# Performance work log

Hardware: AMD Instinct MI355X
Metric: run time of the kernel (lower is better)

## Reference

```python
import jax, jax.numpy as jnp
import numpy as np

DIM = 256
NUM_HEADS = 8
CHUNK = 64
EPS = 1e-5


def layernorm(x, g, b):
    m = jnp.mean(x, axis=-1, keepdims=True)
    v = jnp.mean((x - m) ** 2, axis=-1, keepdims=True)
    return (x - m) / jnp.sqrt(v + EPS) * g + b


def setup_inputs() -> dict:
    key = jax.random.key(0)
    ks = jax.random.split(key, 12)
    B, C, H, W = 8, DIM, 64, 64
    s = 1.0 / np.sqrt(C)
    return {
        "x": jax.random.normal(ks[0], (B, C, H, W), jnp.float32),
        "CVA_input": jax.random.normal(ks[1], (B, C, H, W), jnp.float32),
        "qn_g": jnp.ones((C,), jnp.float32), "qn_b": jnp.zeros((C,), jnp.float32),
        "kn_g": jnp.ones((C,), jnp.float32), "kn_b": jnp.zeros((C,), jnp.float32),
        "vn_g": jnp.ones((C,), jnp.float32), "vn_b": jnp.zeros((C,), jnp.float32),
        "Wq": jax.random.normal(ks[2], (C, C), jnp.float32) * s,
        "bq": jnp.zeros((C,), jnp.float32),
        "Wk": jax.random.normal(ks[3], (C, C), jnp.float32) * s,
        "bk": jnp.zeros((C,), jnp.float32),
        "Wv": jax.random.normal(ks[4], (C, C), jnp.float32) * s,
        "bv": jnp.zeros((C,), jnp.float32),
        "Wp": jax.random.normal(ks[5], (C, C), jnp.float32) * s,
        "bp": jnp.zeros((C,), jnp.float32),
    }


def reference(x, CVA_input, qn_g, qn_b, kn_g, kn_b, vn_g, vn_b,
              Wq, bq, Wk, bk, Wv, bv, Wp, bp):
    B, C, H, W = x.shape
    N = H * W
    nh = NUM_HEADS
    hd = C // nh
    scale = hd ** -0.5
    nc = N // CHUNK  # number of non-overlapping chunks

    xs = x.reshape(B, C, N).transpose(0, 2, 1)          # [B,N,C]
    cva = CVA_input.reshape(B, -1, C)                    # [B,N,C] (raw reshape, as in torch)

    def heads(t):  # [B,N,C] -> [B,nh,nc,CHUNK,hd]
        return t.reshape(B, N, nh, hd).transpose(0, 2, 1, 3).reshape(B, nh, nc, CHUNK, hd)

    q = heads(layernorm(cva, qn_g, qn_b) @ Wq + bq)
    k = heads(layernorm(cva, kn_g, kn_b) @ Wk + bk)
    v = heads(layernorm(xs, vn_g, vn_b) @ Wv + bv)

    # block-local attention: each chunk attends only within itself
    scores = jnp.einsum('bhncd,bhnkd->bhnck', q, k) * scale  # [B,nh,nc,CHUNK,CHUNK]
    probs = jax.nn.softmax(scores, axis=-1)
    o = jnp.einsum('bhnck,bhnkd->bhncd', probs, v)           # [B,nh,nc,CHUNK,hd]

    o = o.reshape(B, nh, N, hd).transpose(0, 2, 1, 3).reshape(B, N, C)
    out = o @ Wp + bp                                        # [B,N,C]
    return out.transpose(0, 2, 1).reshape(B, C, H, W)
```

## Files before the change

### kernel.cpp

```cpp
#include <hip/hip_runtime.h>
#include <hip/hip_bf16.h>

#define NTOK 4096
#define BATCH 8
#define NROWS (BATCH * NTOK)

typedef __attribute__((ext_vector_type(8))) short bfx8;
typedef __attribute__((ext_vector_type(4))) short bfx4;
typedef __attribute__((ext_vector_type(4))) float f32x4;

__device__ __forceinline__ short f2bf(float f) {
    unsigned u = __builtin_bit_cast(unsigned, f);
    u += 0x7fffu + ((u >> 16) & 1u);
    return (short)(u >> 16);
}
__device__ __forceinline__ unsigned pk2(float a, float b) {
    return (unsigned)(unsigned short)f2bf(a) | ((unsigned)(unsigned short)f2bf(b) << 16);
}

#define MFMA16(a, b, c) __builtin_amdgcn_mfma_f32_16x16x32_bf16(a, b, c, 0, 0, 0)
#define LGKM0()                                              \
    do {                                                     \
        asm volatile("s_waitcnt lgkmcnt(0)" ::: "memory");   \
        __builtin_amdgcn_sched_barrier(0);                   \
    } while (0)

__global__ __launch_bounds__(256) void prep_w(
    const float* __restrict__ Wq, const float* __restrict__ Wk,
    const float* __restrict__ Wv, const float* __restrict__ Wp,
    const float* __restrict__ qg, const float* __restrict__ qb,
    const float* __restrict__ kg, const float* __restrict__ kb,
    const float* __restrict__ vg, const float* __restrict__ vb,
    short* __restrict__ wt, float* __restrict__ bbp) {
    int m = blockIdx.x;
    int ci0 = blockIdx.y * 16;
    const float *W, *g, *be;
    float scale = 1.0f;
    if (m == 0)      { W = Wq; g = qg; be = qb; scale = 0.17677669529663687f; }
    else if (m == 1) { W = Wk; g = kg; be = kb; }
    else if (m == 2) { W = Wv; g = vg; be = vb; }
    else             { W = Wp; g = nullptr; be = nullptr; }
    __shared__ float tile[16][257];
    int t = threadIdx.x;
#pragma unroll
    for (int i = 0; i < 16; i++)
        tile[i][t] = W[(size_t)(ci0 + i) * 256 + t];
    __syncthreads();
    float p = 0.f;
    if (be) {
#pragma unroll
        for (int i = 0; i < 16; i++) p += be[ci0 + i] * tile[i][t];
    }
    bbp[(m * 16 + blockIdx.y) * 256 + t] = p;
    short* WT = wt + m * 65536 + t * 256 + ci0;
    bfx8 o0, o1;
#pragma unroll
    for (int j = 0; j < 8; j++) {
        float gv = g ? g[ci0 + j] : 1.0f;
        o0[j] = f2bf(scale * gv * tile[j][t]);
    }
#pragma unroll
    for (int j = 0; j < 8; j++) {
        float gv = g ? g[ci0 + 8 + j] : 1.0f;
        o1[j] = f2bf(scale * gv * tile[8 + j][t]);
    }
    *reinterpret_cast<bfx8*>(WT) = o0;
    *reinterpret_cast<bfx8*>(WT + 8) = o1;
}

__global__ __launch_bounds__(256) void prep_b(
    const float* __restrict__ bq, const float* __restrict__ bk,
    const float* __restrict__ bv, const float* __restrict__ bp,
    const float* __restrict__ bbp, float* __restrict__ bb) {
    int m = blockIdx.x, t = threadIdx.x;
    const float* bias = (m == 0) ? bq : (m == 1) ? bk : (m == 2) ? bv : bp;
    float scale = (m == 0) ? 0.17677669529663687f : 1.0f;
    float s = bias[t];
#pragma unroll
    for (int i = 0; i < 16; i++) s += bbp[(m * 16 + i) * 256 + t];
    bb[m * 256 + t] = scale * s;
}

__global__ __launch_bounds__(512, 4) void mega(const float* __restrict__ x,
                                               const float* __restrict__ cva,
                                               const short* __restrict__ wt,
                                               const float* __restrict__ bb,
                                               float* __restrict__ out) {
    int id = blockIdx.x;
    int b = id >> 6, ch = id & 63;
    int t = threadIdx.x, w = t >> 6, l = t & 63, c = l & 15, g = l >> 4;

    __shared__ short A[64 * 264];
    __shared__ short scr_[8][2560];
    __shared__ float red[8][64][2];
    short* S = scr_[w];

    const float* xb   = x + (size_t)b * 1048576 + ch * 64;
    const float* cvab = cva + (size_t)(b * 4096 + ch * 64) * 256;

    {
        int r16 = l >> 4;
        float fv[2][16];
#pragma unroll
        for (int p2 = 0; p2 < 2; p2++) {
            int row = w * 8 + p2 * 4 + r16;
#pragma unroll
            for (int i = 0; i < 4; i++) {
                float4 v4 = *reinterpret_cast<const float4*>(
                    cvab + (size_t)row * 256 + c * 16 + i * 4);
                fv[p2][i * 4 + 0] = v4.x;
                fv[p2][i * 4 + 1] = v4.y;
                fv[p2][i * 4 + 2] = v4.z;
                fv[p2][i * 4 + 3] = v4.w;
            }
        }
#pragma unroll
        for (int p2 = 0; p2 < 2; p2++) {
            int row = w * 8 + p2 * 4 + r16;
            float s = 0.f, q2 = 0.f;
#pragma unroll
            for (int i = 0; i < 16; i++) {
                s += fv[p2][i];
                q2 += fv[p2][i] * fv[p2][i];
            }
            s += __shfl_xor(s, 1);  q2 += __shfl_xor(q2, 1);
            s += __shfl_xor(s, 2);  q2 += __shfl_xor(q2, 2);
            s += __shfl_xor(s, 4);  q2 += __shfl_xor(q2, 4);
            s += __shfl_xor(s, 8);  q2 += __shfl_xor(q2, 8);
            float mean = s * (1.0f / 256.0f);
            float rstd = rsqrtf(q2 * (1.0f / 256.0f) - mean * mean + 1e-5f);
            bfx8 o0, o1;
#pragma unroll
            for (int jj = 0; jj < 8; jj++) {
                o0[jj] = f2bf((fv[p2][jj] - mean) * rstd);
                o1[jj] = f2bf((fv[p2][8 + jj] - mean) * rstd);
            }
            *reinterpret_cast<bfx8*>(A + row * 264 + c * 16) = o0;
            *reinterpret_cast<bfx8*>(A + row * 264 + c * 16 + 8) = o1;
        }
    }
    __syncthreads();

    f32x4 qa[4][2] = {}, ka[4][2] = {};
    {
        const short* wq0 = wt + (size_t)(w * 32 + c) * 256 + g * 8;
        const short* wq1 = wq0 + 16 * 256;
        const short* wk0 = wq0 + 65536;
        const short* wk1 = wq1 + 65536;
#pragma unroll
        for (int ks = 0; ks < 8; ks++) {
            bfx8 af[4];
#pragma unroll
            for (int m = 0; m < 4; m++)
                af[m] = *reinterpret_cast<const bfx8*>(A + (m * 16 + c) * 264 + ks * 32 + g * 8);
            bfx8 q0 = *reinterpret_cast<const bfx8*>(wq0 + ks * 32);
            bfx8 q1 = *reinterpret_cast<const bfx8*>(wq1 + ks * 32);
            bfx8 k0 = *reinterpret_cast<const bfx8*>(wk0 + ks * 32);
            bfx8 k1 = *reinterpret_cast<const bfx8*>(wk1 + ks * 32);
#pragma unroll
            for (int m = 0; m < 4; m++) {
                qa[m][0] = MFMA16(af[m], q0, qa[m][0]);
                qa[m][1] = MFMA16(af[m], q1, qa[m][1]);
                ka[m][0] = MFMA16(af[m], k0, ka[m][0]);
                ka[m][1] = MFMA16(af[m], k1, ka[m][1]);
            }
        }
    }

    float xg[32];
#pragma unroll
    for (int i = 0; i < 32; i++) xg[i] = xb[(size_t)(w * 32 + i) * 4096 + l];

    bfx8 qf[4];
    {
        float b0 = bb[w * 32 + c], b1 = bb[w * 32 + 16 + c];
#pragma unroll
        for (int m = 0; m < 4; m++)
#pragma unroll
            for (int j = 0; j < 4; j++) {
                S[(m * 16 + g * 4 + j) * 40 + c]      = f2bf(qa[m][0][j] + b0);
                S[(m * 16 + g * 4 + j) * 40 + 16 + c] = f2bf(qa[m][1][j] + b1);
            }
        LGKM0();
#pragma unroll
        for (int np = 0; np < 4; np++)
            qf[np] = *reinterpret_cast<const bfx8*>(S + (np * 16 + c) * 40 + g * 8);
        LGKM0();
    }

    bfx8 kf[4];
    {
        float b0 = bb[256 + w * 32 + c], b1 = bb[256 + w * 32 + 16 + c];
#pragma unroll
        for (int m = 0; m < 4; m++)
#pragma unroll
            for (int j = 0; j < 4; j++) {
                S[(m * 16 + g * 4 + j) * 40 + c]      = f2bf(ka[m][0][j] + b0);
                S[(m * 16 + g * 4 + j) * 40 + 16 + c] = f2bf(ka[m][1][j] + b1);
            }
        LGKM0();
#pragma unroll
        for (int m = 0; m < 4; m++)
            kf[m] = *reinterpret_cast<const bfx8*>(S + (m * 16 + c) * 40 + g * 8);
        LGKM0();
    }

    {
        float s = 0.f, q2 = 0.f;
#pragma unroll
        for (int i = 0; i < 32; i++) { s += xg[i]; q2 += xg[i] * xg[i]; }
        red[w][l][0] = s;
        red[w][l][1] = q2;
    }
    __syncthreads();

    float xmean, xrstd;
    {
        float s = 0.f, q2 = 0.f;
#pragma unroll
        for (int j2 = 0; j2 < 8; j2++) { s += red[j2][l][0]; q2 += red[j2][l][1]; }
        xmean = s * (1.0f / 256.0f);
        xrstd = rsqrtf(q2 * (1.0f / 256.0f) - xmean * xmean + 1e-5f);
    }

#pragma unroll
    for (int i2 = 0; i2 < 4; i2++) {
        bfx8 o;
#pragma unroll
        for (int jj = 0; jj < 8; jj++) o[jj] = f2bf((xg[i2 * 8 + jj] - xmean) * xrstd);
        *reinterpret_cast<bfx8*>(A + l * 264 + w * 32 + i2 * 8) = o;
    }
    __syncthreads();

    f32x4 sa[4][4] = {};
#pragma unroll
    for (int m = 0; m < 4; m++)
#pragma unroll
        for (int np = 0; np < 4; np++)
            sa[m][np] = MFMA16(kf[m], qf[np], sa[m][np]);

    float rs[4];
#pragma unroll
    for (int np = 0; np < 4; np++) {
        float mx = sa[0][np][0];
#pragma unroll
        for (int m = 0; m < 4; m++)
#pragma unroll
            for (int j = 0; j < 4; j++) mx = fmaxf(mx, sa[m][np][j]);
        mx = fmaxf(mx, __shfl_xor(mx, 16));
        mx = fmaxf(mx, __shfl_xor(mx, 32));
        float sum = 0.f;
#pragma unroll
        for (int m = 0; m < 4; m++)
#pragma unroll
            for (int j = 0; j < 4; j++) {
                float e = __expf(sa[m][np][j] - mx);
                sa[m][np][j] = e;
                sum += e;
            }
        sum += __shfl_xor(sum, 16);
        sum += __shfl_xor(sum, 32);
        rs[np] = 1.0f / sum;
    }

    unsigned Pp[4][4][2];
#pragma unroll
    for (int m = 0; m < 4; m++)
#pragma unroll
        for (int np = 0; np < 4; np++) {
            Pp[m][np][0] = pk2(sa[m][np][0], sa[m][np][1]);
            Pp[m][np][1] = pk2(sa[m][np][2], sa[m][np][3]);
        }

    f32x4 va[4][2] = {};
    {
        const short* w0 = wt + 2 * 65536 + (size_t)(w * 32 + c) * 256 + g * 8;
        const short* w1 = w0 + 16 * 256;
#pragma unroll
        for (int ks = 0; ks < 8; ks++) {
            bfx8 af[4];
#pragma unroll
            for (int m = 0; m < 4; m++)
                af[m] = *reinterpret_cast<const bfx8*>(A + (m * 16 + c) * 264 + ks * 32 + g * 8);
            bfx8 v0 = *reinterpret_cast<const bfx8*>(w0 + ks * 32);
            bfx8 v1 = *reinterpret_cast<const bfx8*>(w1 + ks * 32);
#pragma unroll
            for (int m = 0; m < 4; m++) {
                va[m][0] = MFMA16(af[m], v0, va[m][0]);
                va[m][1] = MFMA16(af[m], v1, va[m][1]);
            }
        }
    }
    __syncthreads();

    bfx8 vf[2][2];
    {
        float b0 = bb[512 + w * 32 + c], b1 = bb[512 + w * 32 + 16 + c];
#pragma unroll
        for (int m = 0; m < 4; m++) {
            bfx4 t0, t1;
#pragma unroll
            for (int j = 0; j < 4; j++) {
                t0[j] = f2bf(va[m][0][j] + b0);
                t1[j] = f2bf(va[m][1][j] + b1);
            }
            *reinterpret_cast<bfx4*>(S + c * 72 + m * 16 + g * 4)        = t0;
            *reinterpret_cast<bfx4*>(S + (16 + c) * 72 + m * 16 + g * 4) = t1;
        }
        LGKM0();
#pragma unroll
        for (int ks = 0; ks < 2; ks++)
#pragma unroll
            for (int mD = 0; mD < 2; mD++)
                vf[ks][mD] = *reinterpret_cast<const bfx8*>(S + (mD * 16 + c) * 72 + ks * 32 + g * 8);
        LGKM0();
    }

    f32x4 oa[2][4] = {};
#pragma unroll
    for (int ks = 0; ks < 2; ks++) {
#pragma unroll
        for (int m2 = 0; m2 < 2; m2++)
#pragma unroll
            for (int np = 0; np < 4; np++) {
                *reinterpret_cast<unsigned*>(S + (np * 16 + c) * 40 + m2 * 16 + g * 4)     = Pp[ks * 2 + m2][np][0];
                *reinterpret_cast<unsigned*>(S + (np * 16 + c) * 40 + m2 * 16 + g * 4 + 2) = Pp[ks * 2 + m2][np][1];
            }
        LGKM0();
        bfx8 pf[4];
#pragma unroll
        for (int np = 0; np < 4; np++)
            pf[np] = *reinterpret_cast<const bfx8*>(S + (np * 16 + c) * 40 + g * 8);
        LGKM0();
#pragma unroll
        for (int mD = 0; mD < 2; mD++)
#pragma unroll
            for (int np = 0; np < 4; np++)
                oa[mD][np] = MFMA16(vf[ks][mD], pf[np], oa[mD][np]);
    }

#pragma unroll
    for (int mD = 0; mD < 2; mD++)
#pragma unroll
        for (int np = 0; np < 4; np++) {
            bfx4 o4;
#pragma unroll
            for (int j = 0; j < 4; j++) o4[j] = f2bf(oa[mD][np][j] * rs[np]);
            *reinterpret_cast<bfx4*>(A + (np * 16 + c) * 264 + w * 32 + mD * 16 + g * 4) = o4;
        }
    __syncthreads();

    {
        f32x4 pa[4][2] = {};
        const short* w0 = wt + 3 * 65536 + (size_t)(w * 32 + c) * 256 + g * 8;
        const short* w1 = w0 + 16 * 256;
#pragma unroll
        for (int ks = 0; ks < 8; ks++) {
            bfx8 af[4];
#pragma unroll
            for (int m = 0; m < 4; m++)
                af[m] = *reinterpret_cast<const bfx8*>(A + (m * 16 + c) * 264 + ks * 32 + g * 8);
            bfx8 p0 = *reinterpret_cast<const bfx8*>(w0 + ks * 32);
            bfx8 p1 = *reinterpret_cast<const bfx8*>(w1 + ks * 32);
#pragma unroll
            for (int m = 0; m < 4; m++) {
                pa[m][0] = MFMA16(af[m], p0, pa[m][0]);
                pa[m][1] = MFMA16(af[m], p1, pa[m][1]);
            }
        }
        float* outb = out + (size_t)b * 1048576 + ch * 64;
#pragma unroll
        for (int p = 0; p < 2; p++) {
            int co = w * 32 + p * 16 + c;
            float bvv = bb[768 + co];
            float* op = outb + (size_t)co * 4096 + g * 4;
#pragma unroll
            for (int m = 0; m < 4; m++) {
                float4 st;
                st.x = pa[m][p][0] + bvv;
                st.y = pa[m][p][1] + bvv;
                st.z = pa[m][p][2] + bvv;
                st.w = pa[m][p][3] + bvv;
                *reinterpret_cast<float4*>(op + m * 16) = st;
            }
        }
    }
}

extern "C" void kernel_launch(void* const* d_in, const int* in_sizes, int n_in,
                              void* d_out, int out_size, void* d_ws, size_t ws_size,
                              hipStream_t stream) {
    const float* x   = (const float*)d_in[0];
    const float* cva = (const float*)d_in[1];
    const float* qg  = (const float*)d_in[2];
    const float* qb  = (const float*)d_in[3];
    const float* kg  = (const float*)d_in[4];
    const float* kb  = (const float*)d_in[5];
    const float* vg  = (const float*)d_in[6];
    const float* vb  = (const float*)d_in[7];
    const float* Wq  = (const float*)d_in[8];
    const float* bq  = (const float*)d_in[9];
    const float* Wk  = (const float*)d_in[10];
    const float* bk  = (const float*)d_in[11];
    const float* Wv  = (const float*)d_in[12];
    const float* bv  = (const float*)d_in[13];
    const float* Wp  = (const float*)d_in[14];
    const float* bp  = (const float*)d_in[15];
    float* out = (float*)d_out;
    char* ws = (char*)d_ws;

    short* wt  = (short*)(ws);
    float* bb  = (float*)(ws + 4 * 65536 * sizeof(short));
    float* bbp = bb + 1024;

    prep_w<<<dim3(4, 16), 256, 0, stream>>>(Wq, Wk, Wv, Wp, qg, qb, kg, kb, vg, vb,
                                            wt, bbp);
    prep_b<<<4, 256, 0, stream>>>(bq, bk, bv, bp, bbp, bb);

    mega<<<512, 512, 0, stream>>>(x, cva, wt, bb, out);
}
```

Baseline: 67.08 us.

## Switch to fp16 MFMA, swizzle LDS tiles, and overlap x load with cva LayerNorm

Converts every operand from bf16 to fp16 and uses the f16 MFMA intrinsic. It also drops the padded LDS rows in favour of XOR-swizzled layouts, adds a separate per-wave xo buffer for the normalized x and the attention output, and reuses A as per-wave scratch. The x loads and their LayerNorm move up alongside the cva LayerNorm, and Q/K/V fragment transposes run in two halves, which shrinks LDS use to raise occupancy and removes one barrier. In exchange, fp16 has a smaller range than bf16, and the element-wise scalar LDS stores may cost more instructions than the old vector stores.

```diff
diff --git a/kernel.cpp b/kernel.cpp
--- a/kernel.cpp
+++ b/kernel.cpp
@@ -5,20 +5,26 @@
 #define BATCH 8
 #define NROWS (BATCH * NTOK)
 
-typedef __attribute__((ext_vector_type(8))) short bfx8;
+typedef __attribute__((ext_vector_type(8))) _Float16 hfx8;
 typedef __attribute__((ext_vector_type(4))) short bfx4;
 typedef __attribute__((ext_vector_type(4))) float f32x4;
 
-__device__ __forceinline__ short f2bf(float f) {
-    unsigned u = __builtin_bit_cast(unsigned, f);
-    u += 0x7fffu + ((u >> 16) & 1u);
-    return (short)(u >> 16);
-}
-__device__ __forceinline__ unsigned pk2(float a, float b) {
-    return (unsigned)(unsigned short)f2bf(a) | ((unsigned)(unsigned short)f2bf(b) << 16);
-}
-
-#define MFMA16(a, b, c) __builtin_amdgcn_mfma_f32_16x16x32_bf16(a, b, c, 0, 0, 0)
+__device__ __forceinline__ short f2h(float f) {
+    _Float16 h = (_Float16)f;
+    return __builtin_bit_cast(short, h);
+}
+__device__ __forceinline__ unsigned pk2h(float a, float b) {
+    return (unsigned)(unsigned short)f2h(a) | ((unsigned)(unsigned short)f2h(b) << 16);
+}
+
+__device__ __forceinline__ int aswz(int row, int col) {
+    return (row * 256 + col) ^ ((row & 7) << 3);
+}
+__device__ __forceinline__ int xoidx(int row, int col) {
+    return row * 32 + ((((col >> 3) + (row >> 1)) & 3) << 3) + (col & 7);
+}
+
+#define MFMA16(a, b, c) __builtin_amdgcn_mfma_f32_16x16x32_f16(a, b, c, 0, 0, 0)
 #define LGKM0()                                              \
     do {                                                     \
         asm volatile("s_waitcnt lgkmcnt(0)" ::: "memory");   \
@@ -53,19 +59,19 @@
     }
     bbp[(m * 16 + blockIdx.y) * 256 + t] = p;
     short* WT = wt + m * 65536 + t * 256 + ci0;
-    bfx8 o0, o1;
+    short o0[8], o1[8];
 #pragma unroll
     for (int j = 0; j < 8; j++) {
         float gv = g ? g[ci0 + j] : 1.0f;
-        o0[j] = f2bf(scale * gv * tile[j][t]);
+        o0[j] = f2h(scale * gv * tile[j][t]);
     }
 #pragma unroll
     for (int j = 0; j < 8; j++) {
         float gv = g ? g[ci0 + 8 + j] : 1.0f;
-        o1[j] = f2bf(scale * gv * tile[8 + j][t]);
-    }
-    *reinterpret_cast<bfx8*>(WT) = o0;
-    *reinterpret_cast<bfx8*>(WT + 8) = o1;
+        o1[j] = f2h(scale * gv * tile[8 + j][t]);
+    }
+#pragma unroll
+    for (int j = 0; j < 8; j++) { WT[j] = o0[j]; WT[8 + j] = o1[j]; }
 }
 
 __global__ __launch_bounds__(256) void prep_b(
@@ -90,16 +96,16 @@
     int b = id >> 6, ch = id & 63;
     int t = threadIdx.x, w = t >> 6, l = t & 63, c = l & 15, g = l >> 4;
 
-    __shared__ short A[64 * 264];
-    __shared__ short scr_[8][2560];
+    __shared__ short A[64 * 256];
+    __shared__ short xo[8][2048];
     __shared__ float red[8][64][2];
-    short* S = scr_[w];
+    short* S = A + w * 2048;
 
     const float* xb   = x + (size_t)b * 1048576 + ch * 64;
     const float* cvab = cva + (size_t)(b * 4096 + ch * 64) * 256;
 
     {
-        int r16 = l >> 4;
+        int r16 = g;
         float fv[2][16];
 #pragma unroll
         for (int p2 = 0; p2 < 2; p2++) {
@@ -114,6 +120,10 @@
                 fv[p2][i * 4 + 3] = v4.w;
             }
         }
+        float xg[32];
+#pragma unroll
+        for (int i = 0; i < 32; i++) xg[i] = xb[(size_t)(w * 32 + i) * 4096 + l];
+
 #pragma unroll
         for (int p2 = 0; p2 < 2; p2++) {
             int row = w * 8 + p2 * 4 + r16;
@@ -129,17 +139,37 @@
             s += __shfl_xor(s, 8);  q2 += __shfl_xor(q2, 8);
             float mean = s * (1.0f / 256.0f);
             float rstd = rsqrtf(q2 * (1.0f / 256.0f) - mean * mean + 1e-5f);
-            bfx8 o0, o1;
+            short o0[8], o1[8];
 #pragma unroll
             for (int jj = 0; jj < 8; jj++) {
-                o0[jj] = f2bf((fv[p2][jj] - mean) * rstd);
-                o1[jj] = f2bf((fv[p2][8 + jj] - mean) * rstd);
-            }
-            *reinterpret_cast<bfx8*>(A + row * 264 + c * 16) = o0;
-            *reinterpret_cast<bfx8*>(A + row * 264 + c * 16 + 8) = o1;
-        }
-    }
-    __syncthreads();
+                o0[jj] = f2h((fv[p2][jj] - mean) * rstd);
+                o1[jj] = f2h((fv[p2][8 + jj] - mean) * rstd);
+            }
+            short* d0 = A + aswz(row, c * 16);
+            short* d1 = A + aswz(row, c * 16 + 8);
+#pragma unroll
+            for (int jj = 0; jj < 8; jj++) { d0[jj] = o0[jj]; d1[jj] = o1[jj]; }
+        }
+
+        float s = 0.f, q2 = 0.f;
+#pragma unroll
+        for (int i = 0; i < 32; i++) { s += xg[i]; q2 += xg[i] * xg[i]; }
+        red[w][l][0] = s;
+        red[w][l][1] = q2;
+        __syncthreads();
+
+        float s2 = 0.f, q22 = 0.f;
+#pragma unroll
+        for (int j2 = 0; j2 < 8; j2++) { s2 += red[j2][l][0]; q22 += red[j2][l][1]; }
+        float xmean = s2 * (1.0f / 256.0f);
+        float xrstd = rsqrtf(q22 * (1.0f / 256.0f) - xmean * xmean + 1e-5f);
+#pragma unroll
+        for (int i2 = 0; i2 < 4; i2++) {
+            short* dd = xo[w] + xoidx(l, i2 * 8);
+#pragma unroll
+            for (int jj = 0; jj < 8; jj++) dd[jj] = f2h((xg[i2 * 8 + jj] - xmean) * xrstd);
+        }
+    }
 
     f32x4 qa[4][2] = {}, ka[4][2] = {};
     {
@@ -149,14 +179,14 @@
         const short* wk1 = wq1 + 65536;
 #pragma unroll
         for (int ks = 0; ks < 8; ks++) {
-            bfx8 af[4];
+            hfx8 af[4];
 #pragma unroll
             for (int m = 0; m < 4; m++)
-                af[m] = *reinterpret_cast<const bfx8*>(A + (m * 16 + c) * 264 + ks * 32 + g * 8);
-            bfx8 q0 = *reinterpret_cast<const bfx8*>(wq0 + ks * 32);
-            bfx8 q1 = *reinterpret_cast<const bfx8*>(wq1 + ks * 32);
-            bfx8 k0 = *reinterpret_cast<const bfx8*>(wk0 + ks * 32);
-            bfx8 k1 = *reinterpret_cast<const bfx8*>(wk1 + ks * 32);
+                af[m] = *reinterpret_cast<const hfx8*>(A + aswz(m * 16 + c, ks * 32 + g * 8));
+            hfx8 q0 = *reinterpret_cast<const hfx8*>(wq0 + ks * 32);
+            hfx8 q1 = *reinterpret_cast<const hfx8*>(wq1 + ks * 32);
+            hfx8 k0 = *reinterpret_cast<const hfx8*>(wk0 + ks * 32);
+            hfx8 k1 = *reinterpret_cast<const hfx8*>(wk1 + ks * 32);
 #pragma unroll
             for (int m = 0; m < 4; m++) {
                 qa[m][0] = MFMA16(af[m], q0, qa[m][0]);
@@ -166,71 +196,48 @@
             }
         }
     }
-
-    float xg[32];
-#pragma unroll
-    for (int i = 0; i < 32; i++) xg[i] = xb[(size_t)(w * 32 + i) * 4096 + l];
-
-    bfx8 qf[4];
+    __syncthreads();
+
+
+    hfx8 qf[4];
     {
         float b0 = bb[w * 32 + c], b1 = bb[w * 32 + 16 + c];
 #pragma unroll
-        for (int m = 0; m < 4; m++)
-#pragma unroll
-            for (int j = 0; j < 4; j++) {
-                S[(m * 16 + g * 4 + j) * 40 + c]      = f2bf(qa[m][0][j] + b0);
-                S[(m * 16 + g * 4 + j) * 40 + 16 + c] = f2bf(qa[m][1][j] + b1);
-            }
-        LGKM0();
-#pragma unroll
-        for (int np = 0; np < 4; np++)
-            qf[np] = *reinterpret_cast<const bfx8*>(S + (np * 16 + c) * 40 + g * 8);
-        LGKM0();
-    }
-
-    bfx8 kf[4];
+        for (int th = 0; th < 2; th++) {
+#pragma unroll
+            for (int m2 = 0; m2 < 2; m2++)
+#pragma unroll
+                for (int j = 0; j < 4; j++) {
+                    S[(m2 * 16 + g * 4 + j) * 40 + c]      = f2h(qa[th * 2 + m2][0][j] + b0);
+                    S[(m2 * 16 + g * 4 + j) * 40 + 16 + c] = f2h(qa[th * 2 + m2][1][j] + b1);
+                }
+            LGKM0();
+#pragma unroll
+            for (int np = 0; np < 2; np++)
+                qf[th * 2 + np] = *reinterpret_cast<const hfx8*>(S + (np * 16 + c) * 40 + g * 8);
+            LGKM0();
+        }
+    }
+
+    hfx8 kf[4];
     {
         float b0 = bb[256 + w * 32 + c], b1 = bb[256 + w * 32 + 16 + c];
 #pragma unroll
-        for (int m = 0; m < 4; m++)
-#pragma unroll
-            for (int j = 0; j < 4; j++) {
-                S[(m * 16 + g * 4 + j) * 40 + c]      = f2bf(ka[m][0][j] + b0);
-                S[(m * 16 + g * 4 + j) * 40 + 16 + c] = f2bf(ka[m][1][j] + b1);
-            }
-        LGKM0();
-#pragma unroll
-        for (int m = 0; m < 4; m++)
-            kf[m] = *reinterpret_cast<const bfx8*>(S + (m * 16 + c) * 40 + g * 8);
-        LGKM0();
-    }
-
-    {
-        float s = 0.f, q2 = 0.f;
-#pragma unroll
-        for (int i = 0; i < 32; i++) { s += xg[i]; q2 += xg[i] * xg[i]; }
-        red[w][l][0] = s;
-        red[w][l][1] = q2;
-    }
-    __syncthreads();
-
-    float xmean, xrstd;
-    {
-        float s = 0.f, q2 = 0.f;
-#pragma unroll
-        for (int j2 = 0; j2 < 8; j2++) { s += red[j2][l][0]; q2 += red[j2][l][1]; }
-        xmean = s * (1.0f / 256.0f);
-        xrstd = rsqrtf(q2 * (1.0f / 256.0f) - xmean * xmean + 1e-5f);
-    }
-
-#pragma unroll
-    for (int i2 = 0; i2 < 4; i2++) {
-        bfx8 o;
-#pragma unroll
-        for (int jj = 0; jj < 8; jj++) o[jj] = f2bf((xg[i2 * 8 + jj] - xmean) * xrstd);
-        *reinterpret_cast<bfx8*>(A + l * 264 + w * 32 + i2 * 8) = o;
-    }
-    __syncthreads();
+        for (int th = 0; th < 2; th++) {
+#pragma unroll
+            for (int m2 = 0; m2 < 2; m2++)
+#pragma unroll
+                for (int j = 0; j < 4; j++) {
+                    S[(m2 * 16 + g * 4 + j) * 40 + c]      = f2h(ka[th * 2 + m2][0][j] + b0);
+                    S[(m2 * 16 + g * 4 + j) * 40 + 16 + c] = f2h(ka[th * 2 + m2][1][j] + b1);
+                }
+            LGKM0();
+#pragma unroll
+            for (int np = 0; np < 2; np++)
+                kf[th * 2 + np] = *reinterpret_cast<const hfx8*>(S + (np * 16 + c) * 40 + g * 8);
+            LGKM0();
+        }
+    }
 
     f32x4 sa[4][4] = {};
 #pragma unroll
@@ -268,8 +275,8 @@
     for (int m = 0; m < 4; m++)
 #pragma unroll
         for (int np = 0; np < 4; np++) {
-            Pp[m][np][0] = pk2(sa[m][np][0], sa[m][np][1]);
-            Pp[m][np][1] = pk2(sa[m][np][2], sa[m][np][3]);
+            Pp[m][np][0] = pk2h(sa[m][np][0], sa[m][np][1]);
+            Pp[m][np][1] = pk2h(sa[m][np][2], sa[m][np][3]);
         }
 
     f32x4 va[4][2] = {};
@@ -278,12 +285,12 @@
         const short* w1 = w0 + 16 * 256;
 #pragma unroll
         for (int ks = 0; ks < 8; ks++) {
-            bfx8 af[4];
+            hfx8 af[4];
 #pragma unroll
             for (int m = 0; m < 4; m++)
-                af[m] = *reinterpret_cast<const bfx8*>(A + (m * 16 + c) * 264 + ks * 32 + g * 8);
-            bfx8 v0 = *reinterpret_cast<const bfx8*>(w0 + ks * 32);
-            bfx8 v1 = *reinterpret_cast<const bfx8*>(w1 + ks * 32);
+                af[m] = *reinterpret_cast<const hfx8*>(xo[ks] + xoidx(m * 16 + c, g * 8));
+            hfx8 v0 = *reinterpret_cast<const hfx8*>(w0 + ks * 32);
+            hfx8 v1 = *reinterpret_cast<const hfx8*>(w1 + ks * 32);
 #pragma unroll
             for (int m = 0; m < 4; m++) {
                 va[m][0] = MFMA16(af[m], v0, va[m][0]);
@@ -291,53 +298,58 @@
             }
         }
     }
+
+    hfx8 vf[2][2];
+    {
+        float b0 = bb[512 + w * 32 + c], b1 = bb[512 + w * 32 + 16 + c];
+#pragma unroll
+        for (int ks = 0; ks < 2; ks++) {
+#pragma unroll
+            for (int m2 = 0; m2 < 2; m2++) {
+                int m = ks * 2 + m2;
+                bfx4 t0, t1;
+#pragma unroll
+                for (int j = 0; j < 4; j++) {
+                    t0[j] = f2h(va[m][0][j] + b0);
+                    t1[j] = f2h(va[m][1][j] + b1);
+                }
+                *reinterpret_cast<bfx4*>(S + c * 40 + m2 * 16 + g * 4)        = t0;
+                *reinterpret_cast<bfx4*>(S + (16 + c) * 40 + m2 * 16 + g * 4) = t1;
+            }
+            LGKM0();
+#pragma unroll
+            for (int mD = 0; mD < 2; mD++)
+                vf[ks][mD] = *reinterpret_cast<const hfx8*>(S + (mD * 16 + c) * 40 + g * 8);
+            LGKM0();
+        }
+    }
+
+    f32x4 oa[2][4] = {};
+#pragma unroll
+    for (int ks = 0; ks < 2; ks++) {
+#pragma unroll
+        for (int th = 0; th < 2; th++) {
+#pragma unroll
+            for (int m2 = 0; m2 < 2; m2++)
+#pragma unroll
+                for (int np = 0; np < 2; np++) {
+                    *reinterpret_cast<unsigned*>(S + (np * 16 + c) * 40 + m2 * 16 + g * 4)     = Pp[ks * 2 + m2][th * 2 + np][0];
+                    *reinterpret_cast<unsigned*>(S + (np * 16 + c) * 40 + m2 * 16 + g * 4 + 2) = Pp[ks * 2 + m2][th * 2 + np][1];
+                }
+            LGKM0();
+            hfx8 pf[2];
+#pragma unroll
+            for (int np = 0; np < 2; np++)
+                pf[np] = *reinterpret_cast<const hfx8*>(S + (np * 16 + c) * 40 + g * 8);
+            LGKM0();
+#pragma unroll
+            for (int mD = 0; mD < 2; mD++)
+#pragma unroll
+                for (int np = 0; np < 2; np++)
+                    oa[mD][th * 2 + np] = MFMA16(vf[ks][mD], pf[np], oa[mD][th * 2 + np]);
+        }
+    }
     __syncthreads();
-
-    bfx8 vf[2][2];
-    {
-        float b0 = bb[512 + w * 32 + c], b1 = bb[512 + w * 32 + 16 + c];
-#pragma unroll
-        for (int m = 0; m < 4; m++) {
-            bfx4 t0, t1;
-#pragma unroll
-            for (int j = 0; j < 4; j++) {
-                t0[j] = f2bf(va[m][0][j] + b0);
-                t1[j] = f2bf(va[m][1][j] + b1);
-            }
-            *reinterpret_cast<bfx4*>(S + c * 72 + m * 16 + g * 4)        = t0;
-            *reinterpret_cast<bfx4*>(S + (16 + c) * 72 + m * 16 + g * 4) = t1;
-        }
-        LGKM0();
-#pragma unroll
-        for (int ks = 0; ks < 2; ks++)
-#pragma unroll
-            for (int mD = 0; mD < 2; mD++)
-                vf[ks][mD] = *reinterpret_cast<const bfx8*>(S + (mD * 16 + c) * 72 + ks * 32 + g * 8);
-        LGKM0();
-    }
-
-    f32x4 oa[2][4] = {};
-#pragma unroll
-    for (int ks = 0; ks < 2; ks++) {
-#pragma unroll
-        for (int m2 = 0; m2 < 2; m2++)
-#pragma unroll
-            for (int np = 0; np < 4; np++) {
-                *reinterpret_cast<unsigned*>(S + (np * 16 + c) * 40 + m2 * 16 + g * 4)     = Pp[ks * 2 + m2][np][0];
-                *reinterpret_cast<unsigned*>(S + (np * 16 + c) * 40 + m2 * 16 + g * 4 + 2) = Pp[ks * 2 + m2][np][1];
-            }
-        LGKM0();
-        bfx8 pf[4];
-#pragma unroll
-        for (int np = 0; np < 4; np++)
-            pf[np] = *reinterpret_cast<const bfx8*>(S + (np * 16 + c) * 40 + g * 8);
-        LGKM0();
-#pragma unroll
-        for (int mD = 0; mD < 2; mD++)
-#pragma unroll
-            for (int np = 0; np < 4; np++)
-                oa[mD][np] = MFMA16(vf[ks][mD], pf[np], oa[mD][np]);
-    }
 
 #pragma unroll
     for (int mD = 0; mD < 2; mD++)
@@ -345,8 +357,8 @@
         for (int np = 0; np < 4; np++) {
             bfx4 o4;
 #pragma unroll
-            for (int j = 0; j < 4; j++) o4[j] = f2bf(oa[mD][np][j] * rs[np]);
-            *reinterpret_cast<bfx4*>(A + (np * 16 + c) * 264 + w * 32 + mD * 16 + g * 4) = o4;
+            for (int j = 0; j < 4; j++) o4[j] = f2h(oa[mD][np][j] * rs[np]);
+            *reinterpret_cast<bfx4*>(xo[w] + xoidx(np * 16 + c, mD * 16 + g * 4)) = o4;
         }
     __syncthreads();
 
@@ -356,12 +368,12 @@
         const short* w1 = w0 + 16 * 256;
 #pragma unroll
         for (int ks = 0; ks < 8; ks++) {
-            bfx8 af[4];
+            hfx8 af[4];
 #pragma unroll
             for (int m = 0; m < 4; m++)
-                af[m] = *reinterpret_cast<const bfx8*>(A + (m * 16 + c) * 264 + ks * 32 + g * 8);
-            bfx8 p0 = *reinterpret_cast<const bfx8*>(w0 + ks * 32);
-            bfx8 p1 = *reinterpret_cast<const bfx8*>(w1 + ks * 32);
+                af[m] = *reinterpret_cast<const hfx8*>(xo[ks] + xoidx(m * 16 + c, g * 8));
+            hfx8 p0 = *reinterpret_cast<const hfx8*>(w0 + ks * 32);
+            hfx8 p1 = *reinterpret_cast<const hfx8*>(w1 + ks * 32);
 #pragma unroll
             for (int m = 0; m < 4; m++) {
                 pa[m][0] = MFMA16(af[m], p0, pa[m][0]);
```

Measured after the change: 67.83 us. About the same (+1.1%).
